# Kernel tuning notes

Hardware: AMD Instinct MI355X
Metric: run time of the kernel (lower is better)

## Reference

```python
import jax, jax.numpy as jnp
import numpy as np

LAMB = 0.1
NEG = -1e30  # safe -inf surrogate (avoids nan in logaddexp chains)


def _ctc_nll(log_probs, labels2d, input_lengths, label_lengths):
    """Standard CTC negative log-likelihood (blank=0) via forward DP.
    log_probs: [B,T,V] log-softmaxed; labels2d: [B,L] padded; lengths: [B].
    """
    B, T, V = log_probs.shape
    L = labels2d.shape[1]
    S = 2 * L + 1  # extended label sequence: blank, l1, blank, l2, ...
    s = jnp.arange(S)
    lab_idx = jnp.minimum(s // 2, L - 1)
    ext = jnp.where((s % 2 == 0)[None, :], 0, labels2d[:, lab_idx])  # [B,S]
    ext_m2 = jnp.concatenate([jnp.full((B, 2), -1, ext.dtype), ext[:, :-2]], axis=1)
    # skip (s-2 -> s) allowed only for non-blank positions with different prev label
    allow = ((s % 2 == 1) & (s >= 2))[None, :] & (ext != ext_m2)  # [B,S]

    # emission log-probs gathered per extended position: [B,T,S]
    ext_b = jnp.broadcast_to(ext[:, None, :], (B, T, S))
    emit = jnp.take_along_axis(log_probs, ext_b, axis=2)

    alpha = jnp.full((B, S), NEG, log_probs.dtype)
    alpha = alpha.at[:, 0].set(emit[:, 0, 0]).at[:, 1].set(emit[:, 0, 1])

    def step(alpha, inp):
        emit_t, t = inp
        a1 = jnp.concatenate([jnp.full((B, 1), NEG, alpha.dtype), alpha[:, :-1]], axis=1)
        a2 = jnp.concatenate([jnp.full((B, 2), NEG, alpha.dtype), alpha[:, :-2]], axis=1)
        a2 = jnp.where(allow, a2, NEG)
        new = jnp.logaddexp(jnp.logaddexp(alpha, a1), a2) + emit_t
        # freeze alpha for sequences that already ended
        new = jnp.where((t < input_lengths)[:, None], new, alpha)
        return new, None

    emits = jnp.swapaxes(emit, 0, 1)[1:]          # [T-1,B,S]
    ts = jnp.arange(1, T)
    alpha, _ = jax.lax.scan(step, alpha, (emits, ts))

    end = 2 * label_lengths                        # final blank position per seq
    a_end = jnp.take_along_axis(alpha, end[:, None], axis=1)[:, 0]
    a_end1 = jnp.take_along_axis(alpha, jnp.maximum(end - 1, 0)[:, None], axis=1)[:, 0]
    return -jnp.logaddexp(a_end, a_end1)           # [B] NLL, warp-ctc convention


def reference(logits, labels, input_lengths, label_lengths):
    B, T, V = logits.shape
    labels2d = labels.reshape(B, -1)
    log_probs = jax.nn.log_softmax(logits, axis=-1)
    costs_ctc = _ctc_nll(log_probs, labels2d, input_lengths, label_lengths)
    # CRF denominator with fully-connected graph: logZ = sum_t logsumexp_v logits
    mask = jnp.arange(T)[None, :] < input_lengths[:, None]
    costs_den = jnp.sum(jnp.where(mask, jax.nn.logsumexp(logits, axis=2), 0.0), axis=1)
    costs_all = costs_den - (1.0 + LAMB) * costs_ctc
    costs = costs_all.sum() / B  # size_average=True
    return costs.reshape(1)


def setup_inputs() -> dict:
    key = jax.random.key(0)
    k1, k2, k3, k4 = jax.random.split(key, 4)
    B, T, V, L = 16, 800, 4000, 100
    logits = jax.random.normal(k1, (B, T, V), dtype=jnp.float32)
    labels = jax.random.randint(k2, (B * L,), 1, V)          # blank=0 excluded
    input_lengths = jax.random.randint(k3, (B,), 400, T + 1)  # >= 2L+1
    label_lengths = jax.random.randint(k4, (B,), 1, L + 1)
    return {"logits": logits, "labels": labels,
            "input_lengths": input_lengths, "label_lengths": label_lengths}
```

## Files before the change

kernel.cpp:

```cpp
#include <hip/hip_runtime.h>
#include <math.h>

constexpr int B = 16, T = 800, V = 4000, L = 100;
constexpr int EST = 104;
constexpr float LAMB = 0.1f;
constexpr float LN2 = 0.6931471805599453f;

typedef float f32x4 __attribute__((ext_vector_type(4)));

__global__ __launch_bounds__(256) void lse_emit_kernel(
        const float* __restrict__ logits, const int* __restrict__ labels,
        float* __restrict__ lse_arr, float* __restrict__ emit_all) {
    const int w = threadIdx.x >> 6, lane = threadIdx.x & 63;
    const int row = blockIdx.x * 4 + w;
    const int b = row / T;
    const float* __restrict__ rp = logits + (size_t)row * V;
    const f32x4* __restrict__ rp4 = (const f32x4*)rp;

    float s0 = 0.f, s1 = 0.f, s2 = 0.f, s3 = 0.f;
    for (int i = lane; i < 1000; i += 64) {
        f32x4 x = __builtin_nontemporal_load(rp4 + i);
        s0 += __expf(fminf(x.x, 80.f));
        s1 += __expf(fminf(x.y, 80.f));
        s2 += __expf(fminf(x.z, 80.f));
        s3 += __expf(fminf(x.w, 80.f));
    }
    float s = (s0 + s1) + (s2 + s3);
    #pragma unroll
    for (int k = 1; k < 64; k <<= 1) s += __shfl_xor(s, k);
    float lse = __logf(s);

    if (lane < L / 2) {
        int2 lab = *(const int2*)(labels + b * L + 2 * lane);
        float2 o = make_float2(__expf(rp[lab.x] - lse),
                               __expf(rp[lab.y] - lse));
        *(float2*)(emit_all + (size_t)row * EST + 2 * lane) = o;
    } else if (lane == 50) {
        emit_all[(size_t)row * EST + 100] = __expf(rp[0] - lse);
    } else if (lane == 51) {
        lse_arr[row] = lse;
    }
}

__device__ __forceinline__ float dpp_shr1(float x) {
    return __int_as_float(__builtin_amdgcn_update_dpp(
        0, __float_as_int(x), 0x138 , 0xF, 0xF, false));
}
__device__ __forceinline__ float wave_max63(float x) {
    int xi;
    xi = __float_as_int(x);
    x = fmaxf(x, __int_as_float(__builtin_amdgcn_update_dpp(xi, xi, 0x111, 0xF, 0xF, false)));
    xi = __float_as_int(x);
    x = fmaxf(x, __int_as_float(__builtin_amdgcn_update_dpp(xi, xi, 0x112, 0xF, 0xF, false)));
    xi = __float_as_int(x);
    x = fmaxf(x, __int_as_float(__builtin_amdgcn_update_dpp(xi, xi, 0x114, 0xF, 0xF, false)));
    xi = __float_as_int(x);
    x = fmaxf(x, __int_as_float(__builtin_amdgcn_update_dpp(xi, xi, 0x118, 0xF, 0xF, false)));
    xi = __float_as_int(x);
    x = fmaxf(x, __int_as_float(__builtin_amdgcn_update_dpp(xi, xi, 0x142, 0xF, 0xF, false)));
    xi = __float_as_int(x);
    x = fmaxf(x, __int_as_float(__builtin_amdgcn_update_dpp(xi, xi, 0x143, 0xF, 0xF, false)));
    return x;
}

#define DPSTEP(Q, R) do {                                            \
    float pa3 = dpp_shr1(a3);                                        \
    float n0 = (a0 + pa3) * (R);                                     \
    float n1 = (a1 + a0 + (allow1 ? pa3 : 0.f)) * (Q).x;             \
    float n2 = (a2 + a1) * (R);                                      \
    float n3 = (a3 + a2 + (allow3 ? a1 : 0.f)) * (Q).y;              \
    a0 = n0; a1 = n1; a2 = n2; a3 = n3; } while (0)

#define REFILL(Q, R, TC) do {                                        \
    int u_ = (TC); u_ = (u_ < len) ? u_ : (len - 1);                 \
    const float* er_ = eA + u_ * EST;                                \
    (Q) = *(const float2*)(er_ + loff);                              \
    (R) = er_[100]; } while (0)

#define RESCALE() do {                                               \
    a0 = v0 ? a0 : 0.f; a1 = v1 ? a1 : 0.f;                          \
    a2 = v2 ? a2 : 0.f; a3 = v3 ? a3 : 0.f;                          \
    float lm_ = fmaxf(fmaxf(a0, a1), fmaxf(a2, a3));                 \
    float wm_ = wave_max63(lm_);                                     \
    int wmb_ = __builtin_amdgcn_readlane(__float_as_int(wm_), 63);   \
    int eb_ = (wmb_ >> 23) & 0xFF;              \
    int hs_ = (100 - (eb_ - 127)) >> 1;        \
    float sc_ = __int_as_float((127 + hs_) << 23);   \
    a0 = (a0 * sc_) * sc_; a1 = (a1 * sc_) * sc_;                    \
    a2 = (a2 * sc_) * sc_; a3 = (a3 * sc_) * sc_;                    \
    esc -= 2 * hs_; } while (0)

__global__ __launch_bounds__(64) void ctc_dp_kernel(
        const float* __restrict__ lse_arr, const float* __restrict__ emit_all,
        const int* __restrict__ labels, const int* __restrict__ in_len,
        const int* __restrict__ lab_len, float* __restrict__ costs) {
    const int b = blockIdx.x;
    const int l = threadIdx.x;
    const int len = in_len[b];
    const int lb = lab_len[b];

    float den = 0.f;
    for (int t = l; t < len; t += 64) den += lse_arr[b * T + t];
    #pragma unroll
    for (int k = 1; k < 64; k <<= 1) den += __shfl_xor(den, k);

    int lab0 = -1, lab1 = -2;
    if (l < L / 2) {
        int2 lab = *(const int2*)(labels + b * L + 2 * l);
        lab0 = lab.x; lab1 = lab.y;
    }
    int labm1 = __shfl_up(lab1, 1);
    const bool allow1 = (l >= 1) && (lab0 != labm1);
    const bool allow3 = (lab1 != lab0);
    const int loff = (l < L / 2) ? 2 * l : 0;
    const int endst = 2 * lb;
    const bool v0 = (4 * l     <= endst);
    const bool v1 = (4 * l + 1 <= endst);
    const bool v2 = (4 * l + 2 <= endst);
    const bool v3 = (4 * l + 3 <= endst);
    const float* __restrict__ eA = emit_all + (size_t)b * T * EST;

    int esc = -60;
    const float BOOST = 0x1p60f;
    float a0 = (l == 0) ? eA[100] * BOOST : 0.f;
    float a1 = (l == 0) ? eA[0]   * BOOST : 0.f;
    float a2 = 0.f, a3 = 0.f;

    float2 q0, q1, q2, q3, q4, q5, q6, q7, q8, q9, q10, q11, q12, q13, q14, q15;
    float  r0, r1, r2, r3, r4, r5, r6, r7, r8, r9, r10, r11, r12, r13, r14, r15;
    REFILL(q0,  r0,  1);  REFILL(q1,  r1,  2);  REFILL(q2,  r2,  3);  REFILL(q3,  r3,  4);
    REFILL(q4,  r4,  5);  REFILL(q5,  r5,  6);  REFILL(q6,  r6,  7);  REFILL(q7,  r7,  8);
    REFILL(q8,  r8,  9);  REFILL(q9,  r9,  10); REFILL(q10, r10, 11); REFILL(q11, r11, 12);
    REFILL(q12, r12, 13); REFILL(q13, r13, 14); REFILL(q14, r14, 15); REFILL(q15, r15, 16);

    int t = 1;
    for (; t + 15 < len; t += 16) {
        DPSTEP(q0, r0); REFILL(q0, r0, t + 16);
        DPSTEP(q1, r1); REFILL(q1, r1, t + 17);
        DPSTEP(q2, r2); REFILL(q2, r2, t + 18);
        DPSTEP(q3, r3); REFILL(q3, r3, t + 19);
        DPSTEP(q4, r4); REFILL(q4, r4, t + 20);
        DPSTEP(q5, r5); REFILL(q5, r5, t + 21);
        DPSTEP(q6, r6); REFILL(q6, r6, t + 22);
        DPSTEP(q7, r7); REFILL(q7, r7, t + 23);
        RESCALE();
        DPSTEP(q8,  r8);  REFILL(q8,  r8,  t + 24);
        DPSTEP(q9,  r9);  REFILL(q9,  r9,  t + 25);
        DPSTEP(q10, r10); REFILL(q10, r10, t + 26);
        DPSTEP(q11, r11); REFILL(q11, r11, t + 27);
        DPSTEP(q12, r12); REFILL(q12, r12, t + 28);
        DPSTEP(q13, r13); REFILL(q13, r13, t + 29);
        DPSTEP(q14, r14); REFILL(q14, r14, t + 30);
        DPSTEP(q15, r15); REFILL(q15, r15, t + 31);
        RESCALE();
    }
    if (t + 7 < len) {
        DPSTEP(q0, r0); DPSTEP(q1, r1); DPSTEP(q2, r2); DPSTEP(q3, r3);
        DPSTEP(q4, r4); DPSTEP(q5, r5); DPSTEP(q6, r6); DPSTEP(q7, r7);
        t += 8; RESCALE();
        if (t < len) { DPSTEP(q8,  r8);  ++t; }
        if (t < len) { DPSTEP(q9,  r9);  ++t; }
        if (t < len) { DPSTEP(q10, r10); ++t; }
        if (t < len) { DPSTEP(q11, r11); ++t; }
        if (t < len) { DPSTEP(q12, r12); ++t; }
        if (t < len) { DPSTEP(q13, r13); ++t; }
        if (t < len) { DPSTEP(q14, r14); ++t; }
    } else {
        if (t < len) { DPSTEP(q0, r0); ++t; }
        if (t < len) { DPSTEP(q1, r1); ++t; }
        if (t < len) { DPSTEP(q2, r2); ++t; }
        if (t < len) { DPSTEP(q3, r3); ++t; }
        if (t < len) { DPSTEP(q4, r4); ++t; }
        if (t < len) { DPSTEP(q5, r5); ++t; }
        if (t < len) { DPSTEP(q6, r6); ++t; }
    }

    __shared__ float sa[256];
    sa[4 * l] = a0; sa[4 * l + 1] = a1; sa[4 * l + 2] = a2; sa[4 * l + 3] = a3;
    __syncthreads();
    if (l == 0) {
        int end = endst;
        float sum = sa[end] + sa[end - 1];
        sum = fmaxf(sum, 1e-37f);
        float nll = -(logf(sum) + (float)esc * LN2);
        costs[b] = den - (1.0f + LAMB) * nll;
    }
}

__global__ void finalize_kernel(const float* __restrict__ costs,
                                float* __restrict__ out) {
    int tid = threadIdx.x;
    float c = (tid < B) ? costs[tid] : 0.f;
    #pragma unroll
    for (int off = 32; off > 0; off >>= 1) c += __shfl_down(c, off, 64);
    if (tid == 0) out[0] = c / (float)B;
}

extern "C" void kernel_launch(void* const* d_in, const int* in_sizes, int n_in,
                              void* d_out, int out_size, void* d_ws, size_t ws_size,
                              hipStream_t stream) {
    const float* logits  = (const float*)d_in[0];
    const int*   labels  = (const int*)d_in[1];
    const int*   in_len  = (const int*)d_in[2];
    const int*   lab_len = (const int*)d_in[3];
    float* out = (float*)d_out;

    float* emit_all = (float*)d_ws;
    float* lse_arr  = emit_all + (size_t)B * T * EST;
    float* costs    = lse_arr + B * T;

    lse_emit_kernel<<<B * T / 4, 256, 0, stream>>>(logits, labels, lse_arr, emit_all);
    ctc_dp_kernel<<<B, 64, 0, stream>>>(lse_arr, emit_all, labels, in_len, lab_len, costs);
    finalize_kernel<<<1, 64, 0, stream>>>(costs, out);
}
```

Baseline: 349.2 us.

## Split CTC DP into producer wave staging emissions via LDS ring buffer

```diff
diff --git a/kernel.cpp b/kernel.cpp
--- a/kernel.cpp
+++ b/kernel.cpp
@@ -70,12 +70,6 @@
     float n2 = (a2 + a1) * (R);                                      \
     float n3 = (a3 + a2 + (allow3 ? a1 : 0.f)) * (Q).y;              \
     a0 = n0; a1 = n1; a2 = n2; a3 = n3; } while (0)
-
-#define REFILL(Q, R, TC) do {                                        \
-    int u_ = (TC); u_ = (u_ < len) ? u_ : (len - 1);                 \
-    const float* er_ = eA + u_ * EST;                                \
-    (Q) = *(const float2*)(er_ + loff);                              \
-    (R) = er_[100]; } while (0)
 
 #define RESCALE() do {                                               \
     a0 = v0 ? a0 : 0.f; a1 = v1 ? a1 : 0.f;                          \
@@ -90,95 +84,148 @@
     a2 = (a2 * sc_) * sc_; a3 = (a3 * sc_) * sc_;                    \
     esc -= 2 * hs_; } while (0)
 
-__global__ __launch_bounds__(64) void ctc_dp_kernel(
+__global__ __launch_bounds__(128) void ctc_dp_kernel(
         const float* __restrict__ lse_arr, const float* __restrict__ emit_all,
         const int* __restrict__ labels, const int* __restrict__ in_len,
         const int* __restrict__ lab_len, float* __restrict__ costs) {
-    const int b = blockIdx.x;
-    const int l = threadIdx.x;
+    __shared__ float smem[32][128];
+    __shared__ float sa[256];
+    const int b   = blockIdx.x;
+    const int tid = threadIdx.x;
+    const int wid = tid >> 6;
+    const int ln  = tid & 63;
     const int len = in_len[b];
-    const int lb = lab_len[b];
+    const int lb  = lab_len[b];
+    const int NT  = len - 1;
+    const int nb  = (NT + 7) >> 3;
 
     float den = 0.f;
-    for (int t = l; t < len; t += 64) den += lse_arr[b * T + t];
+    for (int t = ln; t < len; t += 64) den += lse_arr[b * T + t];
     #pragma unroll
     for (int k = 1; k < 64; k <<= 1) den += __shfl_xor(den, k);
 
     int lab0 = -1, lab1 = -2;
-    if (l < L / 2) {
-        int2 lab = *(const int2*)(labels + b * L + 2 * l);
+    if (ln < L / 2) {
+        int2 lab = *(const int2*)(labels + b * L + 2 * ln);
         lab0 = lab.x; lab1 = lab.y;
     }
     int labm1 = __shfl_up(lab1, 1);
-    const bool allow1 = (l >= 1) && (lab0 != labm1);
+    const bool allow1 = (ln >= 1) && (lab0 != labm1);
     const bool allow3 = (lab1 != lab0);
-    const int loff = (l < L / 2) ? 2 * l : 0;
+    const int loff = (ln < L / 2) ? 2 * ln : 0;
     const int endst = 2 * lb;
-    const bool v0 = (4 * l     <= endst);
-    const bool v1 = (4 * l + 1 <= endst);
-    const bool v2 = (4 * l + 2 <= endst);
-    const bool v3 = (4 * l + 3 <= endst);
+    const bool v0 = (4 * ln     <= endst);
+    const bool v1 = (4 * ln + 1 <= endst);
+    const bool v2 = (4 * ln + 2 <= endst);
+    const bool v3 = (4 * ln + 3 <= endst);
     const float* __restrict__ eA = emit_all + (size_t)b * T * EST;
 
     int esc = -60;
     const float BOOST = 0x1p60f;
-    float a0 = (l == 0) ? eA[100] * BOOST : 0.f;
-    float a1 = (l == 0) ? eA[0]   * BOOST : 0.f;
+    float a0 = (ln == 0) ? eA[100] * BOOST : 0.f;
+    float a1 = (ln == 0) ? eA[0]   * BOOST : 0.f;
     float a2 = 0.f, a3 = 0.f;
 
-    float2 q0, q1, q2, q3, q4, q5, q6, q7, q8, q9, q10, q11, q12, q13, q14, q15;
-    float  r0, r1, r2, r3, r4, r5, r6, r7, r8, r9, r10, r11, r12, r13, r14, r15;
-    REFILL(q0,  r0,  1);  REFILL(q1,  r1,  2);  REFILL(q2,  r2,  3);  REFILL(q3,  r3,  4);
-    REFILL(q4,  r4,  5);  REFILL(q5,  r5,  6);  REFILL(q6,  r6,  7);  REFILL(q7,  r7,  8);
-    REFILL(q8,  r8,  9);  REFILL(q9,  r9,  10); REFILL(q10, r10, 11); REFILL(q11, r11, 12);
-    REFILL(q12, r12, 13); REFILL(q13, r13, 14); REFILL(q14, r14, 15); REFILL(q15, r15, 16);
-
-    int t = 1;
-    for (; t + 15 < len; t += 16) {
-        DPSTEP(q0, r0); REFILL(q0, r0, t + 16);
-        DPSTEP(q1, r1); REFILL(q1, r1, t + 17);
-        DPSTEP(q2, r2); REFILL(q2, r2, t + 18);
-        DPSTEP(q3, r3); REFILL(q3, r3, t + 19);
-        DPSTEP(q4, r4); REFILL(q4, r4, t + 20);
-        DPSTEP(q5, r5); REFILL(q5, r5, t + 21);
-        DPSTEP(q6, r6); REFILL(q6, r6, t + 22);
-        DPSTEP(q7, r7); REFILL(q7, r7, t + 23);
-        RESCALE();
-        DPSTEP(q8,  r8);  REFILL(q8,  r8,  t + 24);
-        DPSTEP(q9,  r9);  REFILL(q9,  r9,  t + 25);
-        DPSTEP(q10, r10); REFILL(q10, r10, t + 26);
-        DPSTEP(q11, r11); REFILL(q11, r11, t + 27);
-        DPSTEP(q12, r12); REFILL(q12, r12, t + 28);
-        DPSTEP(q13, r13); REFILL(q13, r13, t + 29);
-        DPSTEP(q14, r14); REFILL(q14, r14, t + 30);
-        DPSTEP(q15, r15); REFILL(q15, r15, t + 31);
-        RESCALE();
-    }
-    if (t + 7 < len) {
-        DPSTEP(q0, r0); DPSTEP(q1, r1); DPSTEP(q2, r2); DPSTEP(q3, r3);
-        DPSTEP(q4, r4); DPSTEP(q5, r5); DPSTEP(q6, r6); DPSTEP(q7, r7);
-        t += 8; RESCALE();
-        if (t < len) { DPSTEP(q8,  r8);  ++t; }
-        if (t < len) { DPSTEP(q9,  r9);  ++t; }
-        if (t < len) { DPSTEP(q10, r10); ++t; }
-        if (t < len) { DPSTEP(q11, r11); ++t; }
-        if (t < len) { DPSTEP(q12, r12); ++t; }
-        if (t < len) { DPSTEP(q13, r13); ++t; }
-        if (t < len) { DPSTEP(q14, r14); ++t; }
-    } else {
-        if (t < len) { DPSTEP(q0, r0); ++t; }
-        if (t < len) { DPSTEP(q1, r1); ++t; }
-        if (t < len) { DPSTEP(q2, r2); ++t; }
-        if (t < len) { DPSTEP(q3, r3); ++t; }
-        if (t < len) { DPSTEP(q4, r4); ++t; }
-        if (t < len) { DPSTEP(q5, r5); ++t; }
-        if (t < len) { DPSTEP(q6, r6); ++t; }
-    }
-
-    __shared__ float sa[256];
-    sa[4 * l] = a0; sa[4 * l + 1] = a1; sa[4 * l + 2] = a2; sa[4 * l + 3] = a3;
+    float pA[16], pB[16];
+    float2 qa[8], qb[8];
+    float  ra[8], rb[8];
+
+    if (wid == 1) {
+        #pragma unroll
+        for (int k = 0; k < 8; ++k) {
+            const float* e0 = eA + (size_t)(1 + k) * EST;
+            pA[2*k] = e0[ln]; pA[2*k+1] = e0[64 + ln];
+            const float* e1 = eA + (size_t)(9 + k) * EST;
+            pB[2*k] = e1[ln]; pB[2*k+1] = e1[64 + ln];
+        }
+        #pragma unroll
+        for (int k = 0; k < 8; ++k) {
+            smem[k][ln]      = pA[2*k]; smem[k][64 + ln]      = pA[2*k+1];
+            smem[8 + k][ln]  = pB[2*k]; smem[8 + k][64 + ln]  = pB[2*k+1];
+        }
+        #pragma unroll
+        for (int k = 0; k < 8; ++k) {
+            const float* e2 = eA + (size_t)(17 + k) * EST;
+            pA[2*k] = e2[ln]; pA[2*k+1] = e2[64 + ln];
+            const float* e3 = eA + (size_t)(25 + k) * EST;
+            pB[2*k] = e3[ln]; pB[2*k+1] = e3[64 + ln];
+        }
+        asm volatile("s_waitcnt lgkmcnt(0)" ::: "memory");
+    }
+    asm volatile("s_barrier" ::: "memory");
+
+    if (wid == 0) {
+        #pragma unroll
+        for (int k = 0; k < 8; ++k) {
+            qa[k] = *(const float2*)&smem[k][loff];
+            ra[k] = smem[k][100];
+        }
+    }
+
+    for (int j = 0; j < nb; ++j) {
+        if (wid == 0) {
+            const int jn = (j + 1 < nb) ? (j + 1) : (nb - 1);
+            const int sb = (jn & 3) * 8;
+            const int t0 = 1 + 8 * j;
+            if ((j & 1) == 0) {
+                #pragma unroll
+                for (int k = 0; k < 8; ++k) {
+                    qb[k] = *(const float2*)&smem[sb + k][loff];
+                    rb[k] = smem[sb + k][100];
+                }
+                #pragma unroll
+                for (int k = 0; k < 8; ++k)
+                    if (t0 + k < len) DPSTEP(qa[k], ra[k]);
+            } else {
+                #pragma unroll
+                for (int k = 0; k < 8; ++k) {
+                    qa[k] = *(const float2*)&smem[sb + k][loff];
+                    ra[k] = smem[sb + k][100];
+                }
+                #pragma unroll
+                for (int k = 0; k < 8; ++k)
+                    if (t0 + k < len) DPSTEP(qb[k], rb[k]);
+            }
+            if (t0 + 7 < len) RESCALE();
+        } else {
+            const int sb = ((j + 2) & 3) * 8;
+            const int mt = 1 + 8 * (j + 2) + 16;
+            if ((j & 1) == 0) {
+                #pragma unroll
+                for (int k = 0; k < 8; ++k) {
+                    smem[sb + k][ln]      = pA[2*k];
+                    smem[sb + k][64 + ln] = pA[2*k+1];
+                }
+                #pragma unroll
+                for (int k = 0; k < 8; ++k) {
+                    int tm = mt + k; tm = (tm <= NT) ? tm : NT;
+                    const float* er = eA + (size_t)tm * EST;
+                    pA[2*k] = er[ln]; pA[2*k+1] = er[64 + ln];
+                }
+            } else {
+                #pragma unroll
+                for (int k = 0; k < 8; ++k) {
+                    smem[sb + k][ln]      = pB[2*k];
+                    smem[sb + k][64 + ln] = pB[2*k+1];
+                }
+                #pragma unroll
+                for (int k = 0; k < 8; ++k) {
+                    int tm = mt + k; tm = (tm <= NT) ? tm : NT;
+                    const float* er = eA + (size_t)tm * EST;
+                    pB[2*k] = er[ln]; pB[2*k+1] = er[64 + ln];
+                }
+            }
+            asm volatile("s_waitcnt lgkmcnt(0)" ::: "memory");
+        }
+        asm volatile("s_barrier" ::: "memory");
+    }
+
+    if (wid == 0) {
+        sa[4 * ln] = a0; sa[4 * ln + 1] = a1;
+        sa[4 * ln + 2] = a2; sa[4 * ln + 3] = a3;
+    }
     __syncthreads();
-    if (l == 0) {
+    if (tid == 0) {
         int end = endst;
         float sum = sa[end] + sa[end - 1];
         sum = fmaxf(sum, 1e-37f);
@@ -210,6 +257,6 @@
     float* costs    = lse_arr + B * T;
 
     lse_emit_kernel<<<B * T / 4, 256, 0, stream>>>(logits, labels, lse_arr, emit_all);
-    ctc_dp_kernel<<<B, 64, 0, stream>>>(lse_arr, emit_all, labels, in_len, lab_len, costs);
+    ctc_dp_kernel<<<B, 128, 0, stream>>>(lse_arr, emit_all, labels, in_len, lab_len, costs);
     finalize_kernel<<<1, 64, 0, stream>>>(costs, out);
 }
```

Result: slower. 362.2 us (+3.7%).
